# Kernel tuning notes

Measured on AMD Instinct MI355X. Metric: run time of the kernel, lower is better.

Reference implementation:

```python
import jax, jax.numpy as jnp
import numpy as np

B, N, FIN, FOUT = 8, 2048, 128, 64
ALPHA = 0.2  # leaky relu negative slope
NEG_INF = -9e15


def setup_inputs() -> dict:
    key = jax.random.key(0)
    k_h, k_adj, k_w, k_a, k_b = jax.random.split(key, 5)
    h = jax.random.normal(k_h, (B, N, FIN), dtype=jnp.float32)
    adj = jax.random.randint(k_adj, (N, N), 0, 2).astype(jnp.int32)
    # learned params (xavier-ish scale)
    W = jax.random.normal(k_w, (FIN, FOUT), dtype=jnp.float32) * (1.414 / np.sqrt(FIN))
    a = jax.random.normal(k_a, (2 * FOUT,), dtype=jnp.float32) * 0.1
    mask = jnp.ones((N, N), dtype=jnp.float32)  # trainable mask, init ones
    bias = jax.random.uniform(k_b, (FOUT,), dtype=jnp.float32,
                              minval=-1.0 / np.sqrt(FOUT), maxval=1.0 / np.sqrt(FOUT))
    return {"h": h, "adj": adj, "W": W, "a": a, "mask": mask, "bias": bias}


def reference(h, adj, W, a, mask, bias):
    # Wh: [B,N,FOUT]
    Wh = jnp.einsum('bnc,cd->bnd', h, W)
    d = Wh.shape[-1]
    # e[b,i,j] = leakyrelu(a1 . Wh_i + a2 . Wh_j)  (avoids the [B,N,N,2d] concat)
    f1 = Wh @ a[:d]   # [B,N]
    f2 = Wh @ a[d:]   # [B,N]
    e = jax.nn.leaky_relu(f1[:, :, None] + f2[:, None, :], negative_slope=ALPHA)  # [B,N,N]
    att = jnp.where(adj[None, :, :] > 0, e, NEG_INF)
    att = jax.nn.softmax(att, axis=-1)
    # dropout p=0.0 -> no-op
    h_prime = jnp.einsum('bnm,bmd->bnd', att * mask[None, :, :], Wh)
    return jax.nn.elu(h_prime) + bias  # concat=True branch with bias
```

## Files before the change

kernel.cpp:

```cpp
#include <hip/hip_runtime.h>
#include <cstdint>

#define BB 8
#define NN 2048
#define FIN 128
#define FOUT 64
#define ALPHA 0.2f

typedef __attribute__((ext_vector_type(8))) short bf16x8;
typedef __attribute__((ext_vector_type(4))) float f32x4;

static __device__ __forceinline__ unsigned short f2bf(float x) {
    union { float f; unsigned int u; } v; v.f = x;
    unsigned int r = (v.u + 0x7FFFu + ((v.u >> 16) & 1u)) >> 16;
    return (unsigned short)r;
}
static __device__ __forceinline__ float bf2f(unsigned short b) {
    union { float f; unsigned int u; } v; v.u = ((unsigned int)b) << 16;
    return v.f;
}
static __device__ __forceinline__ unsigned int pack2bf(float lo, float hi) {
    union { float f; unsigned int u; } a, c; a.f = lo; c.f = hi;
    return __builtin_amdgcn_perm(c.u + 0x8000u, a.u + 0x8000u, 0x07060302u);
}

__global__ __launch_bounds__(256) void k_prep(const int* __restrict__ adj,
                                              const float* __restrict__ mask,
                                              unsigned short* __restrict__ gmT) {
    const int i = blockIdx.y;
    const int j = blockIdx.x * 256 + threadIdx.x;
    const int av = adj[(size_t)i * NN + j];
    const float mv = mask[(size_t)i * NN + j];
    const float g = (av > 0) ? mv : 0.f;
    gmT[((size_t)(j >> 5) * NN + i) * 32 + (j & 31)] = f2bf(g);
}

__global__ __launch_bounds__(256) void k_wh(const float* __restrict__ h,
                                            const float* __restrict__ W,
                                            const float* __restrict__ a,
                                            unsigned short* __restrict__ WhTt,
                                            float* __restrict__ f1,
                                            float* __restrict__ f2) {
    __shared__ float hs[64 * 132];
    __shared__ float Ws[FIN * FOUT];
    __shared__ float as_[2 * FOUT];
    __shared__ float Whs[64 * 65];

    const int t  = threadIdx.x;
    const int n0 = blockIdx.x * 64;
    const int b  = blockIdx.y;

    {
        const float* hb = h + ((size_t)b * NN + n0) * FIN;
        #pragma unroll
        for (int q = 0; q < 8; ++q) {
            int f = t + 256 * q;
            int row = f >> 5, c4 = f & 31;
            *(float4*)(&hs[row * 132 + c4 * 4]) =
                *(const float4*)(hb + row * FIN + c4 * 4);
        }
        #pragma unroll
        for (int q = 0; q < 8; ++q) {
            int f = t + 256 * q;
            *(float4*)(&Ws[f * 4]) = *(const float4*)(W + f * 4);
        }
        if (t < 2 * FOUT) as_[t] = a[t];
    }
    __syncthreads();

    const int ti = t >> 4;
    const int td = t & 15;
    float acc[4][4];
    #pragma unroll
    for (int r = 0; r < 4; ++r)
        #pragma unroll
        for (int x = 0; x < 4; ++x) acc[r][x] = 0.f;

    #pragma unroll 4
    for (int c = 0; c < FIN; ++c) {
        float4 wv = *(const float4*)(&Ws[c * FOUT + td * 4]);
        #pragma unroll
        for (int r = 0; r < 4; ++r) {
            float hv = hs[(ti * 4 + r) * 132 + c];
            acc[r][0] += hv * wv.x;
            acc[r][1] += hv * wv.y;
            acc[r][2] += hv * wv.z;
            acc[r][3] += hv * wv.w;
        }
    }

    #pragma unroll
    for (int r = 0; r < 4; ++r) {
        int row = ti * 4 + r;
        Whs[row * 65 + td * 4 + 0] = acc[r][0];
        Whs[row * 65 + td * 4 + 1] = acc[r][1];
        Whs[row * 65 + td * 4 + 2] = acc[r][2];
        Whs[row * 65 + td * 4 + 3] = acc[r][3];
    }
    __syncthreads();

    {
        int rowid = t >> 1, jbl = rowid >> 6, d = rowid & 63, half = t & 1;
        union { bf16x8 v; unsigned int u4[4]; } P0, P1;
        #pragma unroll
        for (int k = 0; k < 4; ++k) {
            int j0 = jbl * 32 + half * 16 + 2 * k;
            P0.u4[k] = pack2bf(Whs[j0 * 65 + d], Whs[(j0 + 1) * 65 + d]);
        }
        #pragma unroll
        for (int k = 0; k < 4; ++k) {
            int j0 = jbl * 32 + half * 16 + 8 + 2 * k;
            P1.u4[k] = pack2bf(Whs[j0 * 65 + d], Whs[(j0 + 1) * 65 + d]);
        }
        unsigned short* dst = WhTt +
            (((size_t)b * 64 + (n0 >> 5) + jbl) * 64 + d) * 32 + half * 16;
        *(bf16x8*)(dst)     = P0.v;
        *(bf16x8*)(dst + 8) = P1.v;
    }

    if (t < 64) {
        float s1 = 0.f, s2 = 0.f;
        #pragma unroll 8
        for (int d = 0; d < FOUT; ++d) {
            float wv = Whs[t * 65 + d];
            s1 += wv * as_[d];
            s2 += wv * as_[FOUT + d];
        }
        f1[(size_t)b * NN + n0 + t] = s1;
        f2[(size_t)b * NN + n0 + t] = s2;
    }
}

__global__ __launch_bounds__(256, 4) void k_attn(const unsigned short* __restrict__ gmT,
                                                 const unsigned short* __restrict__ WhTt,
                                                 const float* __restrict__ f1,
                                                 const float* __restrict__ f2,
                                                 const float* __restrict__ bias,
                                                 float* __restrict__ out) {
    __shared__ float accs[4 * 16 * 66];
    __shared__ float zl[4 * 16];
    __shared__ float red[4];

    const int t    = threadIdx.x;
    const int lane = t & 63;
    const int w    = t >> 6;
    const int m    = lane & 15;
    const int q4   = lane >> 4;
    const int i0   = blockIdx.x * 16;
    const int b    = blockIdx.y;

    const float* f2b = f2 + (size_t)b * NN;
    float lmax = -3.4e38f;
    #pragma unroll
    for (int q = 0; q < NN / 256; ++q)
        lmax = fmaxf(lmax, f2b[t + 256 * q]);
    #pragma unroll
    for (int off = 32; off > 0; off >>= 1)
        lmax = fmaxf(lmax, __shfl_xor(lmax, off));
    if (lane == 0) red[w] = lmax;

    const float f1v = f1[(size_t)b * NN + i0 + m];
    float f1m = f1v;
    #pragma unroll
    for (int off = 8; off > 0; off >>= 1)
        f1m = fmaxf(f1m, __shfl_xor(f1m, off));
    __syncthreads();

    float mb;
    {
        float m2 = fmaxf(fmaxf(red[0], red[1]), fmaxf(red[2], red[3]));
        float s  = f1m + m2;
        mb = fmaxf(s, ALPHA * s);
    }
    const float F1p  = f1v - mb;
    const float F1pp = ALPHA * f1v - mb;

    f32x4 acc0 = {0,0,0,0}, acc1 = {0,0,0,0}, acc2 = {0,0,0,0}, acc3 = {0,0,0,0};
    float zp = 0.f;

    const unsigned short* gA = gmT + ((size_t)(w * 16) * NN + i0 + m) * 32 + q4 * 8;
    const unsigned short* bB = WhTt + (((size_t)b * 64 + w * 16) * 64 + m) * 32 + q4 * 8;
    const float*          fp = f2b + w * 512 + q4 * 8;

    bf16x8 ga, B0, B1, B2, B3;
    float4 fa, fb;
    ga = *(const bf16x8*)(gA);
    B0 = *(const bf16x8*)(bB);
    B1 = *(const bf16x8*)(bB + 512);
    B2 = *(const bf16x8*)(bB + 1024);
    B3 = *(const bf16x8*)(bB + 1536);
    fa = *(const float4*)(fp);
    fb = *(const float4*)(fp + 4);

    #pragma unroll
    for (int st = 0; st < 16; ++st) {
        bf16x8 gan = *(const bf16x8*)(gA + (size_t)(st + 1) * NN * 32);
        const unsigned short* bp = bB + (size_t)(st + 1) * 2048;
        bf16x8 B0n = *(const bf16x8*)(bp);
        bf16x8 B1n = *(const bf16x8*)(bp + 512);
        bf16x8 B2n = *(const bf16x8*)(bp + 1024);
        bf16x8 B3n = *(const bf16x8*)(bp + 1536);
        float4 fan = *(const float4*)(fp + (st + 1) * 32);
        float4 fbn = *(const float4*)(fp + (st + 1) * 32 + 4);

        float pmv[8];
        #pragma unroll
        for (int u = 0; u < 8; ++u) {
            float fv  = (u < 4) ? ((const float*)&fa)[u] : ((const float*)&fb)[u - 4];
            float gmf = bf2f((unsigned short)ga[u]);
            float s1  = F1p + fv;
            float s2  = fmaf(fv, ALPHA, F1pp);
            float p   = __expf(fmaxf(s1, s2));
            float pm  = p * gmf;
            zp += pm;
            pmv[u] = pm;
        }
        union { bf16x8 v; unsigned int u4[4]; } A;
        A.u4[0] = pack2bf(pmv[0], pmv[1]);
        A.u4[1] = pack2bf(pmv[2], pmv[3]);
        A.u4[2] = pack2bf(pmv[4], pmv[5]);
        A.u4[3] = pack2bf(pmv[6], pmv[7]);

        acc0 = __builtin_amdgcn_mfma_f32_16x16x32_bf16(A.v, B0, acc0, 0, 0, 0);
        acc1 = __builtin_amdgcn_mfma_f32_16x16x32_bf16(A.v, B1, acc1, 0, 0, 0);
        acc2 = __builtin_amdgcn_mfma_f32_16x16x32_bf16(A.v, B2, acc2, 0, 0, 0);
        acc3 = __builtin_amdgcn_mfma_f32_16x16x32_bf16(A.v, B3, acc3, 0, 0, 0);

        ga = gan; B0 = B0n; B1 = B1n; B2 = B2n; B3 = B3n; fa = fan; fb = fbn;
    }

    zp += __shfl_xor(zp, 16);
    zp += __shfl_xor(zp, 32);
    if (lane < 16) zl[w * 16 + m] = zp;

    #pragma unroll
    for (int r = 0; r < 4; ++r) {
        int il = q4 * 4 + r;
        accs[(w * 16 + il) * 66 +  0 + m] = acc0[r];
        accs[(w * 16 + il) * 66 + 16 + m] = acc1[r];
        accs[(w * 16 + il) * 66 + 32 + m] = acc2[r];
        accs[(w * 16 + il) * 66 + 48 + m] = acc3[r];
    }
    __syncthreads();

    {
        const int i = t >> 4, d4 = t & 15;
        float zt = zl[i] + zl[16 + i] + zl[32 + i] + zl[48 + i];
        float rz = 1.0f / zt;
        float s0 = 0, s1 = 0, s2 = 0, s3 = 0;
        #pragma unroll
        for (int ww = 0; ww < 4; ++ww) {
            const float* p = &accs[(ww * 16 + i) * 66 + d4 * 4];
            s0 += p[0]; s1 += p[1]; s2 += p[2]; s3 += p[3];
        }
        float4 bv = *(const float4*)(bias + d4 * 4);
        float h0 = s0 * rz, h1 = s1 * rz, h2 = s2 * rz, h3 = s3 * rz;
        float4 o;
        o.x = (h0 > 0.f ? h0 : __expf(h0) - 1.f) + bv.x;
        o.y = (h1 > 0.f ? h1 : __expf(h1) - 1.f) + bv.y;
        o.z = (h2 > 0.f ? h2 : __expf(h2) - 1.f) + bv.z;
        o.w = (h3 > 0.f ? h3 : __expf(h3) - 1.f) + bv.w;
        *(float4*)(out + ((size_t)b * NN + i0 + i) * FOUT + d4 * 4) = o;
    }
}

extern "C" void kernel_launch(void* const* d_in, const int* in_sizes, int n_in,
                              void* d_out, int out_size, void* d_ws, size_t ws_size,
                              hipStream_t stream) {
    const float* h    = (const float*)d_in[0];
    const int*   adj  = (const int*)  d_in[1];
    const float* W    = (const float*)d_in[2];
    const float* a    = (const float*)d_in[3];
    const float* mask = (const float*)d_in[4];
    const float* bias = (const float*)d_in[5];
    float* out = (float*)d_out;

    unsigned short* gmT  = (unsigned short*)d_ws;
    unsigned short* WhTt = gmT + (size_t)(NN / 32) * NN * 32;
    float* f2 = (float*)(WhTt + (size_t)BB * 64 * 64 * 32);
    float* f1 = f2 + (size_t)BB * NN;

    k_prep<<<dim3(NN / 256, NN), 256, 0, stream>>>(adj, mask, gmT);
    k_wh  <<<dim3(NN / 64, BB),  256, 0, stream>>>(h, W, a, WhTt, f1, f2);
    k_attn<<<dim3(NN / 16, BB),  256, 0, stream>>>(gmT, WhTt, f1, f2, bias, out);
}
```

Measured before the change: 123.1 us.

## Vectorize mask prep, fuse f2 max via atomics, compute softmax sum with MFMA

The adjacency/mask prep kernel now reads 8 elements per thread with vector loads and writes one packed 16-byte bf16 store, replacing scattered 2-byte stores. The per-batch max of f2 is computed in the Wh kernel with a wave reduction and an order-preserving atomicMax, so the attention kernel no longer re-reduces all of f2 or needs a block barrier before the main loop. The softmax denominator is accumulated by an extra MFMA against a ones vector instead of scalar adds and shuffles. Operand prefetch is deepened to two stages. This adds an atomic dependency and a reset in the prep kernel, and the deeper prefetch reads further past the last tile.

Result: slower. 126.3 us (+2.6%).

```diff
diff --git a/kernel.cpp b/kernel.cpp
--- a/kernel.cpp
+++ b/kernel.cpp
@@ -23,16 +23,37 @@
     union { float f; unsigned int u; } a, c; a.f = lo; c.f = hi;
     return __builtin_amdgcn_perm(c.u + 0x8000u, a.u + 0x8000u, 0x07060302u);
 }
+static __device__ __forceinline__ unsigned int mapf(float f) {
+    unsigned int b = __float_as_uint(f);
+    return (b & 0x80000000u) ? ~b : (b | 0x80000000u);
+}
+static __device__ __forceinline__ float unmapf(unsigned int u) {
+    return __uint_as_float((u & 0x80000000u) ? (u ^ 0x80000000u) : ~u);
+}
 
 __global__ __launch_bounds__(256) void k_prep(const int* __restrict__ adj,
                                               const float* __restrict__ mask,
-                                              unsigned short* __restrict__ gmT) {
-    const int i = blockIdx.y;
-    const int j = blockIdx.x * 256 + threadIdx.x;
-    const int av = adj[(size_t)i * NN + j];
-    const float mv = mask[(size_t)i * NN + j];
-    const float g = (av > 0) ? mv : 0.f;
-    gmT[((size_t)(j >> 5) * NN + i) * 32 + (j & 31)] = f2bf(g);
+                                              unsigned short* __restrict__ gmT,
+                                              unsigned int* __restrict__ f2maxU) {
+    const int t  = threadIdx.x;
+    const int jb = blockIdx.x;
+    const int i  = blockIdx.y * 64 + (t >> 2);
+    const int jo = (t & 3) * 8;
+    const size_t src = (size_t)i * NN + jb * 32 + jo;
+
+    int4   a0 = *(const int4*)(adj + src);
+    int4   a1 = *(const int4*)(adj + src + 4);
+    float4 m0 = *(const float4*)(mask + src);
+    float4 m1 = *(const float4*)(mask + src + 4);
+
+    union { bf16x8 v; unsigned int u4[4]; } P;
+    P.u4[0] = pack2bf(a0.x > 0 ? m0.x : 0.f, a0.y > 0 ? m0.y : 0.f);
+    P.u4[1] = pack2bf(a0.z > 0 ? m0.z : 0.f, a0.w > 0 ? m0.w : 0.f);
+    P.u4[2] = pack2bf(a1.x > 0 ? m1.x : 0.f, a1.y > 0 ? m1.y : 0.f);
+    P.u4[3] = pack2bf(a1.z > 0 ? m1.z : 0.f, a1.w > 0 ? m1.w : 0.f);
+    *(bf16x8*)(gmT + ((size_t)jb * NN + i) * 32 + jo) = P.v;
+
+    if (blockIdx.x == 0 && blockIdx.y == 0 && t < BB) f2maxU[t] = 0u;
 }
 
 __global__ __launch_bounds__(256) void k_wh(const float* __restrict__ h,
@@ -40,7 +61,8 @@
                                             const float* __restrict__ a,
                                             unsigned short* __restrict__ WhTt,
                                             float* __restrict__ f1,
-                                            float* __restrict__ f2) {
+                                            float* __restrict__ f2,
+                                            unsigned int* __restrict__ f2maxU) {
     __shared__ float hs[64 * 132];
     __shared__ float Ws[FIN * FOUT];
     __shared__ float as_[2 * FOUT];
@@ -128,6 +150,11 @@
         }
         f1[(size_t)b * NN + n0 + t] = s1;
         f2[(size_t)b * NN + n0 + t] = s2;
+        float s2m = s2;
+        #pragma unroll
+        for (int off = 32; off > 0; off >>= 1)
+            s2m = fmaxf(s2m, __shfl_xor(s2m, off));
+        if (t == 0) atomicMax(f2maxU + b, mapf(s2m));
     }
 }
 
@@ -135,11 +162,11 @@
                                                  const unsigned short* __restrict__ WhTt,
                                                  const float* __restrict__ f1,
                                                  const float* __restrict__ f2,
+                                                 const unsigned int* __restrict__ f2maxU,
                                                  const float* __restrict__ bias,
                                                  float* __restrict__ out) {
     __shared__ float accs[4 * 16 * 66];
-    __shared__ float zl[4 * 16];
-    __shared__ float red[4];
+    __shared__ float zl[64];
 
     const int t    = threadIdx.x;
     const int lane = t & 63;
@@ -149,71 +176,55 @@
     const int i0   = blockIdx.x * 16;
     const int b    = blockIdx.y;
 
-    const float* f2b = f2 + (size_t)b * NN;
-    float lmax = -3.4e38f;
-    #pragma unroll
-    for (int q = 0; q < NN / 256; ++q)
-        lmax = fmaxf(lmax, f2b[t + 256 * q]);
-    #pragma unroll
-    for (int off = 32; off > 0; off >>= 1)
-        lmax = fmaxf(lmax, __shfl_xor(lmax, off));
-    if (lane == 0) red[w] = lmax;
-
+    const float f2m = unmapf(f2maxU[b]);
     const float f1v = f1[(size_t)b * NN + i0 + m];
     float f1m = f1v;
     #pragma unroll
     for (int off = 8; off > 0; off >>= 1)
         f1m = fmaxf(f1m, __shfl_xor(f1m, off));
-    __syncthreads();
-
-    float mb;
-    {
-        float m2 = fmaxf(fmaxf(red[0], red[1]), fmaxf(red[2], red[3]));
-        float s  = f1m + m2;
-        mb = fmaxf(s, ALPHA * s);
-    }
+    float sb = f1m + f2m;
+    const float mb   = fmaxf(sb, ALPHA * sb);
     const float F1p  = f1v - mb;
     const float F1pp = ALPHA * f1v - mb;
 
     f32x4 acc0 = {0,0,0,0}, acc1 = {0,0,0,0}, acc2 = {0,0,0,0}, acc3 = {0,0,0,0};
-    float zp = 0.f;
-
+    f32x4 accz = {0,0,0,0};
+    bf16x8 onesB;
+    #pragma unroll
+    for (int u = 0; u < 8; ++u) onesB[u] = (short)0x3F80;
+
+    const float* f2b = f2 + (size_t)b * NN;
     const unsigned short* gA = gmT + ((size_t)(w * 16) * NN + i0 + m) * 32 + q4 * 8;
     const unsigned short* bB = WhTt + (((size_t)b * 64 + w * 16) * 64 + m) * 32 + q4 * 8;
     const float*          fp = f2b + w * 512 + q4 * 8;
 
-    bf16x8 ga, B0, B1, B2, B3;
-    float4 fa, fb;
-    ga = *(const bf16x8*)(gA);
-    B0 = *(const bf16x8*)(bB);
-    B1 = *(const bf16x8*)(bB + 512);
-    B2 = *(const bf16x8*)(bB + 1024);
-    B3 = *(const bf16x8*)(bB + 1536);
-    fa = *(const float4*)(fp);
-    fb = *(const float4*)(fp + 4);
+    bf16x8 gaS[2], B0S[2], B1S[2], B2S[2], B3S[2];
+    float4 faS[2], fbS[2];
+    #pragma unroll
+    for (int s = 0; s < 2; ++s) {
+        gaS[s] = *(const bf16x8*)(gA + (size_t)s * NN * 32);
+        const unsigned short* bp = bB + (size_t)s * 2048;
+        B0S[s] = *(const bf16x8*)(bp);
+        B1S[s] = *(const bf16x8*)(bp + 512);
+        B2S[s] = *(const bf16x8*)(bp + 1024);
+        B3S[s] = *(const bf16x8*)(bp + 1536);
+        faS[s] = *(const float4*)(fp + s * 32);
+        fbS[s] = *(const float4*)(fp + s * 32 + 4);
+    }
 
     #pragma unroll
     for (int st = 0; st < 16; ++st) {
-        bf16x8 gan = *(const bf16x8*)(gA + (size_t)(st + 1) * NN * 32);
-        const unsigned short* bp = bB + (size_t)(st + 1) * 2048;
-        bf16x8 B0n = *(const bf16x8*)(bp);
-        bf16x8 B1n = *(const bf16x8*)(bp + 512);
-        bf16x8 B2n = *(const bf16x8*)(bp + 1024);
-        bf16x8 B3n = *(const bf16x8*)(bp + 1536);
-        float4 fan = *(const float4*)(fp + (st + 1) * 32);
-        float4 fbn = *(const float4*)(fp + (st + 1) * 32 + 4);
-
+        const int cur = st & 1;
         float pmv[8];
         #pragma unroll
         for (int u = 0; u < 8; ++u) {
-            float fv  = (u < 4) ? ((const float*)&fa)[u] : ((const float*)&fb)[u - 4];
-            float gmf = bf2f((unsigned short)ga[u]);
+            float fv  = (u < 4) ? ((const float*)&faS[cur])[u]
+                                : ((const float*)&fbS[cur])[u - 4];
+            float gmf = bf2f((unsigned short)gaS[cur][u]);
             float s1  = F1p + fv;
             float s2  = fmaf(fv, ALPHA, F1pp);
             float p   = __expf(fmaxf(s1, s2));
-            float pm  = p * gmf;
-            zp += pm;
-            pmv[u] = pm;
+            pmv[u] = p * gmf;
         }
         union { bf16x8 v; unsigned int u4[4]; } A;
         A.u4[0] = pack2bf(pmv[0], pmv[1]);
@@ -221,18 +232,26 @@
         A.u4[2] = pack2bf(pmv[4], pmv[5]);
         A.u4[3] = pack2bf(pmv[6], pmv[7]);
 
-        acc0 = __builtin_amdgcn_mfma_f32_16x16x32_bf16(A.v, B0, acc0, 0, 0, 0);
-        acc1 = __builtin_amdgcn_mfma_f32_16x16x32_bf16(A.v, B1, acc1, 0, 0, 0);
-        acc2 = __builtin_amdgcn_mfma_f32_16x16x32_bf16(A.v, B2, acc2, 0, 0, 0);
-        acc3 = __builtin_amdgcn_mfma_f32_16x16x32_bf16(A.v, B3, acc3, 0, 0, 0);
-
-        ga = gan; B0 = B0n; B1 = B1n; B2 = B2n; B3 = B3n; fa = fan; fb = fbn;
-    }
-
-    zp += __shfl_xor(zp, 16);
-    zp += __shfl_xor(zp, 32);
-    if (lane < 16) zl[w * 16 + m] = zp;
-
+        acc0 = __builtin_amdgcn_mfma_f32_16x16x32_bf16(A.v, B0S[cur], acc0, 0, 0, 0);
+        acc1 = __builtin_amdgcn_mfma_f32_16x16x32_bf16(A.v, B1S[cur], acc1, 0, 0, 0);
+        acc2 = __builtin_amdgcn_mfma_f32_16x16x32_bf16(A.v, B2S[cur], acc2, 0, 0, 0);
+        acc3 = __builtin_amdgcn_mfma_f32_16x16x32_bf16(A.v, B3S[cur], acc3, 0, 0, 0);
+        accz = __builtin_amdgcn_mfma_f32_16x16x32_bf16(A.v, onesB,    accz, 0, 0, 0);
+
+        gaS[cur] = *(const bf16x8*)(gA + (size_t)(st + 2) * NN * 32);
+        const unsigned short* bp = bB + (size_t)(st + 2) * 2048;
+        B0S[cur] = *(const bf16x8*)(bp);
+        B1S[cur] = *(const bf16x8*)(bp + 512);
+        B2S[cur] = *(const bf16x8*)(bp + 1024);
+        B3S[cur] = *(const bf16x8*)(bp + 1536);
+        faS[cur] = *(const float4*)(fp + (st + 2) * 32);
+        fbS[cur] = *(const float4*)(fp + (st + 2) * 32 + 4);
+    }
+
+    if (m == 0) {
+        #pragma unroll
+        for (int r = 0; r < 4; ++r) zl[w * 16 + q4 * 4 + r] = accz[r];
+    }
     #pragma unroll
     for (int r = 0; r < 4; ++r) {
         int il = q4 * 4 + r;
@@ -279,8 +298,9 @@
     unsigned short* WhTt = gmT + (size_t)(NN / 32) * NN * 32;
     float* f2 = (float*)(WhTt + (size_t)BB * 64 * 64 * 32);
     float* f1 = f2 + (size_t)BB * NN;
-
-    k_prep<<<dim3(NN / 256, NN), 256, 0, stream>>>(adj, mask, gmT);
-    k_wh  <<<dim3(NN / 64, BB),  256, 0, stream>>>(h, W, a, WhTt, f1, f2);
-    k_attn<<<dim3(NN / 16, BB),  256, 0, stream>>>(gmT, WhTt, f1, f2, bias, out);
-}
+    unsigned int* f2maxU = (unsigned int*)(f1 + (size_t)BB * NN);
+
+    k_prep<<<dim3(64, NN / 64), 256, 0, stream>>>(adj, mask, gmT, f2maxU);
+    k_wh  <<<dim3(NN / 64, BB), 256, 0, stream>>>(h, W, a, WhTt, f1, f2, f2maxU);
+    k_attn<<<dim3(NN / 16, BB), 256, 0, stream>>>(gmT, WhTt, f1, f2, f2maxU, bias, out);
+}
```
